# Optimization experiments

Hardware: AMD Instinct MI355X
Metric: run time of the kernel (lower is better)

The kernel has to match this reference:

```python
import jax, jax.numpy as jnp
import numpy as np

D_MODEL = 1024
N_HEADS = 16
D_HIDDEN = 4096
EPS = 1e-6
MASK_VAL = 1e10


def layernorm(x, gamma, beta):
    # Matches torch module: unbiased std (N-1), divide by (std + eps)
    mean = jnp.mean(x, axis=-1, keepdims=True)
    d = x.shape[-1]
    std = jnp.sqrt(jnp.sum((x - mean) ** 2, axis=-1, keepdims=True) / (d - 1))
    return gamma * (x - mean) / (std + EPS) + beta


def multihead(q_in, k_in, v_in, wq, wk, wv, wo, causal):
    # nn.Linear(bias=False): y = x @ W.T
    q = q_in @ wq.T
    k = k_in @ wk.T
    v = v_in @ wv.T
    B, Sq, D = q.shape
    Sk = k.shape[1]
    H, dh = N_HEADS, D // N_HEADS
    q = q.reshape(B, Sq, H, dh)
    k = k.reshape(B, Sk, H, dh)
    v = v.reshape(B, Sk, H, dh)
    scores = jnp.einsum('bqhd,bkhd->bhqk', q, k)  # [B,H,Sq,Sk]
    if causal:
        tri = jnp.triu(jnp.full((Sk, Sk), MASK_VAL, dtype=scores.dtype), k=1)
        scores = scores - tri  # mask applied BEFORE scaling, as in source
    scale = jnp.sqrt(jnp.asarray(D_MODEL, dtype=scores.dtype))  # d_key = d_model
    att = jax.nn.softmax(scores / scale, axis=-1)
    out = jnp.einsum('bhqk,bkhd->bqhd', att, v).reshape(B, Sq, D)
    return out @ wo.T


def setup_inputs() -> dict:
    key = jax.random.key(0)
    ks = jax.random.split(key, 24)
    B, S, D, DH = 2, 2048, D_MODEL, D_HIDDEN
    w = lambda k, shp: (jax.random.normal(k, shp, dtype=jnp.float32) * 0.02)
    inp = {
        'x': jax.random.normal(ks[0], (B, S, D), dtype=jnp.float32),
        'encoding': jax.random.normal(ks[1], (B, S, D), dtype=jnp.float32),
        'sa_wq': w(ks[2], (D, D)), 'sa_wk': w(ks[3], (D, D)),
        'sa_wv': w(ks[4], (D, D)), 'sa_wo': w(ks[5], (D, D)),
        'ca_wq': w(ks[6], (D, D)), 'ca_wk': w(ks[7], (D, D)),
        'ca_wv': w(ks[8], (D, D)), 'ca_wo': w(ks[9], (D, D)),
        'ff_w1': w(ks[10], (DH, D)), 'ff_b1': jnp.zeros((DH,), jnp.float32),
        'ff_w2': w(ks[11], (D, DH)), 'ff_b2': jnp.zeros((D,), jnp.float32),
        'ln1_g': jnp.ones((D,), jnp.float32), 'ln1_b': jnp.zeros((D,), jnp.float32),
        'ln2_g': jnp.ones((D,), jnp.float32), 'ln2_b': jnp.zeros((D,), jnp.float32),
        'ln3_g': jnp.ones((D,), jnp.float32), 'ln3_b': jnp.zeros((D,), jnp.float32),
    }
    return inp


def reference(x, encoding, sa_wq, sa_wk, sa_wv, sa_wo, ca_wq, ca_wk, ca_wv, ca_wo,
              ff_w1, ff_b1, ff_w2, ff_b2, ln1_g, ln1_b, ln2_g, ln2_b, ln3_g, ln3_b):
    # self-attention (causal) + post-norm residual
    h = layernorm(x + multihead(x, x, x, sa_wq, sa_wk, sa_wv, sa_wo, causal=True), ln1_g, ln1_b)
    # cross-attention + post-norm residual
    h = layernorm(h + multihead(h, encoding, encoding, ca_wq, ca_wk, ca_wv, ca_wo, causal=False), ln2_g, ln2_b)
    # feed-forward + post-norm residual
    ff = jax.nn.relu(h @ ff_w1.T + ff_b1) @ ff_w2.T + ff_b2
    return layernorm(h + ff, ln3_g, ln3_b)
```

## Files before the change

### kernel.cpp

```cpp
#include <hip/hip_runtime.h>
#include <hip/hip_bf16.h>
#include <math.h>

#define D_MODEL 1024
#define NHEADS  16
#define DHEAD   64
#define D_HID   4096

typedef __attribute__((ext_vector_type(8))) short short8;
typedef __attribute__((ext_vector_type(4))) short short4v;
typedef __attribute__((ext_vector_type(4))) float f32x4;
typedef __attribute__((ext_vector_type(16))) float f32x16;

#define QSCALE_F 0.04508422002778011f
#define MASK_T   4.5084220e8f

__device__ inline short f2bs(float x) {
    union { __hip_bfloat16 b; short s; } u;
    u.b = __float2bfloat16(x);
    return u.s;
}
__device__ inline float bs2f(ushort s) {
    union { unsigned u; float f; } v; v.u = ((unsigned)s) << 16; return v.f;
}
__device__ inline unsigned cvtpk(float lo, float hi) {
    unsigned r;
    asm("v_cvt_pk_bf16_f32 %0, %1, %2" : "=v"(r) : "v"(lo), "v"(hi));
    return r;
}
__device__ inline short8 pack8(float4 x, float4 y) {
    short8 v;
    v[0] = f2bs(x.x); v[1] = f2bs(x.y); v[2] = f2bs(x.z); v[3] = f2bs(x.w);
    v[4] = f2bs(y.x); v[5] = f2bs(y.y); v[6] = f2bs(y.z); v[7] = f2bs(y.w);
    return v;
}
typedef const unsigned __attribute__((address_space(1))) gu32;
typedef unsigned __attribute__((address_space(3))) lu32;
__device__ inline void gload16(const void* g, void* l) {
    __builtin_amdgcn_global_load_lds((gu32*)g, (lu32*)l, 16, 0, 0);
}
__device__ inline int swz(int r, int byteInRow) {
    return (r * 128 + byteInRow) ^ ((r & 7) << 4);
}

struct WP { const float* p[10]; };
__global__ __launch_bounds__(256) void cast_weights(WP wp, short* __restrict__ dst) {
    const int n8 = (16 << 20) / 8;
    for (int i = blockIdx.x * 256 + threadIdx.x; i < n8; i += gridDim.x * 256) {
        size_t e = (size_t)i * 8;
        int seg = (int)(e >> 20);
        const float* src;
        if (seg < 8)       src = wp.p[seg] + (e & ((1u << 20) - 1));
        else if (seg < 12) src = wp.p[8] + (e - ((size_t)8 << 20));
        else               src = wp.p[9] + (e - ((size_t)12 << 20));
        float4 a = *(const float4*)src;
        float4 b = *(const float4*)(src + 4);
        *(short8*)(dst + e) = pack8(a, b);
    }
}

__global__ __launch_bounds__(256) void cast_f2b(const float* __restrict__ in,
                                                short* __restrict__ out, int n8) {
    for (int i = blockIdx.x * 256 + threadIdx.x; i < n8; i += gridDim.x * 256) {
        float4 a = *(const float4*)(in + (size_t)i * 8);
        float4 b = *(const float4*)(in + (size_t)i * 8 + 4);
        *(short8*)(out + (size_t)i * 8) = pack8(a, b);
    }
}

template<int OM, bool BIAS, bool RELU, bool ACCUM>
__global__ __launch_bounds__(256) void gemm_mfma(
    const short* __restrict__ A, int lda,
    const short* __restrict__ Bm, int ldb,
    const float* __restrict__ bias,
    float* __restrict__ Cf, short* __restrict__ Cb, int ldc,
    int M, int N, int K, size_t routeElems, float qscale)
{
    __shared__ short Als[128 * 64];
    __shared__ short Bls[128 * 64];

    const int tid = threadIdx.x, w = tid >> 6, l = tid & 63;
    const int l15 = l & 15, lhi = l >> 4;
    const int wr = w >> 1, wc = w & 1;

    const int kh = (OM == 3) ? blockIdx.z : 0;
    if (OM == 3) {
        A  += (size_t)kh * K;
        Bm += (size_t)kh * K;
    }

    const unsigned nwg  = gridDim.x * gridDim.y;
    const unsigned wgid = blockIdx.y * gridDim.x + blockIdx.x;
    const unsigned cpx  = nwg >> 3;
    const unsigned sid  = (wgid & 7) * cpx + (wgid >> 3);
    const int bm = (int)(sid / gridDim.x) * 128;
    const int bn = (int)(sid % gridDim.x) * 128;

    const int srow = w * 8 + (l >> 3);
    const int schk = ((l & 7) ^ (l >> 3)) * 8;

    f32x4 acc[4][4] = {};

    for (int k0 = 0; k0 < K; k0 += 64) {
        #pragma unroll
        for (int i = 0; i < 4; ++i) {
            const short* ga = A  + (size_t)(bm + i * 32 + srow) * lda + k0 + schk;
            const short* gb = Bm + (size_t)(bn + i * 32 + srow) * ldb + k0 + schk;
            gload16(ga, &Als[i * 2048 + w * 512]);
            gload16(gb, &Bls[i * 2048 + w * 512]);
        }
        __syncthreads();

        short8 af[4][2], bf[4][2];
        #pragma unroll
        for (int m = 0; m < 4; ++m) {
            const int row = wr * 64 + m * 16 + l15;
            #pragma unroll
            for (int kk = 0; kk < 2; ++kk)
                af[m][kk] = *(const short8*)&Als[row * 64 + (((kk * 4 + lhi) ^ (l15 & 7)) * 8)];
        }
        #pragma unroll
        for (int n = 0; n < 4; ++n) {
            const int row = wc * 64 + n * 16 + l15;
            #pragma unroll
            for (int kk = 0; kk < 2; ++kk)
                bf[n][kk] = *(const short8*)&Bls[row * 64 + (((kk * 4 + lhi) ^ (l15 & 7)) * 8)];
        }
        #pragma unroll
        for (int kk = 0; kk < 2; ++kk)
            #pragma unroll
            for (int m = 0; m < 4; ++m)
                #pragma unroll
                for (int n = 0; n < 4; ++n)
                    acc[m][n] = __builtin_amdgcn_mfma_f32_16x16x32_bf16(af[m][kk], bf[n][kk], acc[m][n], 0, 0, 0);
        __syncthreads();
    }

    #pragma unroll
    for (int n = 0; n < 4; ++n) {
        const int col = bn + wc * 64 + n * 16 + l15;
        float bv = 0.f;
        if (BIAS && (OM != 3 || kh == 0)) bv = bias[col];
        const float sc = (OM == 2) ? (col < 1024 ? qscale : 1.f) : qscale;
        #pragma unroll
        for (int m = 0; m < 4; ++m) {
            const int row0 = bm + wr * 64 + m * 16 + lhi * 4;
            #pragma unroll
            for (int i = 0; i < 4; ++i) {
                float v = acc[m][n][i] + bv;
                if (ACCUM) v += Cf[(size_t)(row0 + i) * ldc + col];
                if (RELU)  v = fmaxf(v, 0.f);
                v *= sc;
                if (OM == 0) {
                    Cf[(size_t)(row0 + i) * ldc + col] = v;
                } else if (OM == 1) {
                    Cb[(size_t)(row0 + i) * ldc + col] = f2bs(v);
                } else if (OM == 2) {
                    Cb[(size_t)(col >> 10) * routeElems +
                       (size_t)(row0 + i) * 1024 + (col & 1023)] = f2bs(v);
                } else {
                    if (kh == 0) Cf[(size_t)(row0 + i) * ldc + col] = v;
                    else         Cb[(size_t)(row0 + i) * ldc + col] = f2bs(v);
                }
            }
        }
    }
}

__global__ __launch_bounds__(256) void v_prep(
    const short* __restrict__ Vb_, short* __restrict__ Vt, int S)
{
    const int t = blockIdx.x, bh = blockIdx.y;
    const int b = bh >> 4, h = bh & 15;
    const int tid = threadIdx.x;
    const int r = tid >> 2, g = tid & 3;
    __shared__ ushort vs[64][65];

    const size_t inrow = ((size_t)b * S + t * 64 + r) * D_MODEL + h * DHEAD;
    const size_t tbase = ((size_t)bh * (S / 64) + t) * 4096;

    short8 v0 = *(const short8*)(Vb_ + inrow + g * 16);
    short8 v1 = *(const short8*)(Vb_ + inrow + g * 16 + 8);
    #pragma unroll
    for (int j = 0; j < 8; ++j) { vs[r][g * 16 + j] = (ushort)v0[j]; vs[r][g * 16 + 8 + j] = (ushort)v1[j]; }
    __syncthreads();
    short8 q0, q1;
    #pragma unroll
    for (int j = 0; j < 8; ++j) {
        q0[j] = (short)vs[g * 16 + j][r];
        q1[j] = (short)vs[g * 16 + 8 + j][r];
    }
    *(short8*)(Vt + tbase + r * 64 + g * 16)     = q0;
    *(short8*)(Vt + tbase + r * 64 + g * 16 + 8) = q1;
}

template<bool CAUSAL>
__global__ __launch_bounds__(256, 3) void attn_v8(
    const short* __restrict__ Qb, const short* __restrict__ Kr,
    const short* __restrict__ Vt, short* __restrict__ PO,
    float* __restrict__ PL, int S)
{
    __shared__ __align__(16) char smem[2 * 16384];

    const int tid = threadIdx.x, w = tid >> 6, l = tid & 63;
    const int l31 = l & 31, hi = l >> 5;
    const int bnd = blockIdx.x >> 1, s = blockIdx.x & 1;
    const int bh = blockIdx.y, b = bh >> 4, h = bh & 15;
    const int qw = bnd * 128 + w * 32;
    const int q  = qw + l31;

    const short* qp = Qb + ((size_t)(b * S + q)) * 1024 + h * 64 + hi * 8;
    short8 bq[4];
    #pragma unroll
    for (int dc = 0; dc < 4; ++dc) bq[dc] = *(const short8*)(qp + dc * 16);

    const short* kbase = Kr + ((size_t)b * S) * 1024 + h * 64;
    const short* vbase = Vt + (size_t)bh * ((S / 64) * 4096);

    f32x16 ot0 = {}, ot1 = {};
    float l_lane = 0.f;

    const int tMax = CAUSAL ? (2 * bnd + 1) : (S / 64 - 1);
    const int sr = tid >> 2, sc = tid & 3;

    short8 gk0, gk1, gv0, gv1;
    {
        const short* kg = kbase + (size_t)(s * 64 + sr) * 1024 + sc * 8;
        const short* vg = vbase + (size_t)s * 4096 + sr * 64 + sc * 8;
        gk0 = *(const short8*)kg;        gk1 = *(const short8*)(kg + 32);
        gv0 = *(const short8*)vg;        gv1 = *(const short8*)(vg + 32);
    }
    {
        char* Kls = smem;            char* Vls = smem + 8192;
        *(short8*)(Kls + swz(sr, sc * 16))      = gk0;
        *(short8*)(Kls + swz(sr, sc * 16 + 64)) = gk1;
        *(short8*)(Vls + swz(sr, sc * 16))      = gv0;
        *(short8*)(Vls + swz(sr, sc * 16 + 64)) = gv1;
    }
    __syncthreads();

    int cur = 0;
    for (int t = s; t <= tMax; t += 2) {
        const bool hasNext = (t + 2 <= tMax);
        if (hasNext) {
            const short* kg = kbase + (size_t)((t + 2) * 64 + sr) * 1024 + sc * 8;
            const short* vg = vbase + (size_t)(t + 2) * 4096 + sr * 64 + sc * 8;
            gk0 = *(const short8*)kg;    gk1 = *(const short8*)(kg + 32);
            gv0 = *(const short8*)vg;    gv1 = *(const short8*)(vg + 32);
        }

        const char* Kls = smem + cur * 16384;
        const char* Vls = Kls + 8192;
        const int kv0 = t * 64;

        if (!(CAUSAL && kv0 > qw + 31)) {
            f32x16 st0 = {}, st1 = {};
            __builtin_amdgcn_s_setprio(1);
            #pragma unroll
            for (int dc = 0; dc < 4; ++dc) {
                short8 a0 = *(const short8*)(Kls + swz(l31,      dc * 32 + hi * 16));
                short8 a1 = *(const short8*)(Kls + swz(32 + l31, dc * 32 + hi * 16));
                st0 = __builtin_amdgcn_mfma_f32_32x32x16_bf16(a0, bq[dc], st0, 0, 0, 0);
                st1 = __builtin_amdgcn_mfma_f32_32x32x16_bf16(a1, bq[dc], st1, 0, 0, 0);
            }
            __builtin_amdgcn_s_setprio(0);

            if (CAUSAL && kv0 + 31 > qw) {
                #pragma unroll
                for (int r = 0; r < 16; ++r) {
                    int kv = kv0 + (r & 3) + 8 * (r >> 2) + 4 * hi;
                    if (kv > q) st0[r] -= MASK_T;
                }
            }
            if (CAUSAL && kv0 + 63 > qw) {
                #pragma unroll
                for (int r = 0; r < 16; ++r) {
                    int kv = kv0 + 32 + (r & 3) + 8 * (r >> 2) + 4 * hi;
                    if (kv > q) st1[r] -= MASK_T;
                }
            }

            union U { unsigned u[4]; short8 s; };
            U c00, c01, c10, c11;
            {
                float p[16];
                #pragma unroll
                for (int r = 0; r < 16; ++r) { p[r] = __builtin_amdgcn_exp2f(st0[r]); l_lane += p[r]; }
                unsigned wd[8], sx[8];
                #pragma unroll
                for (int i = 0; i < 8; ++i) wd[i] = cvtpk(p[2 * i], p[2 * i + 1]);
                #pragma unroll
                for (int i = 0; i < 8; ++i) sx[i] = __shfl_xor(wd[i], 32, 64);
                if (hi == 0) {
                    c00.u[0] = wd[0]; c00.u[1] = wd[1]; c00.u[2] = sx[0]; c00.u[3] = sx[1];
                    c01.u[0] = wd[4]; c01.u[1] = wd[5]; c01.u[2] = sx[4]; c01.u[3] = sx[5];
                } else {
                    c00.u[0] = sx[2]; c00.u[1] = sx[3]; c00.u[2] = wd[2]; c00.u[3] = wd[3];
                    c01.u[0] = sx[6]; c01.u[1] = sx[7]; c01.u[2] = wd[6]; c01.u[3] = wd[7];
                }
            }
            {
                float p[16];
                #pragma unroll
                for (int r = 0; r < 16; ++r) { p[r] = __builtin_amdgcn_exp2f(st1[r]); l_lane += p[r]; }
                unsigned wd[8], sx[8];
                #pragma unroll
                for (int i = 0; i < 8; ++i) wd[i] = cvtpk(p[2 * i], p[2 * i + 1]);
                #pragma unroll
                for (int i = 0; i < 8; ++i) sx[i] = __shfl_xor(wd[i], 32, 64);
                if (hi == 0) {
                    c10.u[0] = wd[0]; c10.u[1] = wd[1]; c10.u[2] = sx[0]; c10.u[3] = sx[1];
                    c11.u[0] = wd[4]; c11.u[1] = wd[5]; c11.u[2] = sx[4]; c11.u[3] = sx[5];
                } else {
                    c10.u[0] = sx[2]; c10.u[1] = sx[3]; c10.u[2] = wd[2]; c10.u[3] = wd[3];
                    c11.u[0] = sx[6]; c11.u[1] = sx[7]; c11.u[2] = wd[6]; c11.u[3] = wd[7];
                }
            }

            __builtin_amdgcn_s_setprio(1);
            short8 av;
            av  = *(const short8*)(Vls + swz(l31,      hi * 16));
            ot0 = __builtin_amdgcn_mfma_f32_32x32x16_bf16(av, c00.s, ot0, 0, 0, 0);
            av  = *(const short8*)(Vls + swz(32 + l31, hi * 16));
            ot1 = __builtin_amdgcn_mfma_f32_32x32x16_bf16(av, c00.s, ot1, 0, 0, 0);
            av  = *(const short8*)(Vls + swz(l31,      32 + hi * 16));
            ot0 = __builtin_amdgcn_mfma_f32_32x32x16_bf16(av, c01.s, ot0, 0, 0, 0);
            av  = *(const short8*)(Vls + swz(32 + l31, 32 + hi * 16));
            ot1 = __builtin_amdgcn_mfma_f32_32x32x16_bf16(av, c01.s, ot1, 0, 0, 0);
            av  = *(const short8*)(Vls + swz(l31,      64 + hi * 16));
            ot0 = __builtin_amdgcn_mfma_f32_32x32x16_bf16(av, c10.s, ot0, 0, 0, 0);
            av  = *(const short8*)(Vls + swz(32 + l31, 64 + hi * 16));
            ot1 = __builtin_amdgcn_mfma_f32_32x32x16_bf16(av, c10.s, ot1, 0, 0, 0);
            av  = *(const short8*)(Vls + swz(l31,      96 + hi * 16));
            ot0 = __builtin_amdgcn_mfma_f32_32x32x16_bf16(av, c11.s, ot0, 0, 0, 0);
            av  = *(const short8*)(Vls + swz(32 + l31, 96 + hi * 16));
            ot1 = __builtin_amdgcn_mfma_f32_32x32x16_bf16(av, c11.s, ot1, 0, 0, 0);
            __builtin_amdgcn_s_setprio(0);
        }

        if (hasNext) {
            char* Kn = smem + (cur ^ 1) * 16384;
            char* Vn = Kn + 8192;
            *(short8*)(Kn + swz(sr, sc * 16))      = gk0;
            *(short8*)(Kn + swz(sr, sc * 16 + 64)) = gk1;
            *(short8*)(Vn + swz(sr, sc * 16))      = gv0;
            *(short8*)(Vn + swz(sr, sc * 16 + 64)) = gv1;
        }
        __syncthreads();
        cur ^= 1;
    }

    const int qc = bnd * 4 + w;
    const size_t c = ((size_t)bh * (S / 32) + qc) * 2 + s;
    float l_tot = l_lane + __shfl_xor(l_lane, 32, 64);
    if (hi == 0) PL[c * 32 + l31] = l_tot;
    short* po = PO + c * 2048 + (size_t)l31 * 64;
    #pragma unroll
    for (int i = 0; i < 8; ++i) {
        int dbase = ((2 * i) & 3) + 8 * (i >> 1) + 4 * hi;
        *(unsigned*)(po + dbase)      = cvtpk(ot0[2 * i], ot0[2 * i + 1]);
        *(unsigned*)(po + 32 + dbase) = cvtpk(ot1[2 * i], ot1[2 * i + 1]);
    }
}

__global__ __launch_bounds__(256) void attn_combine(
    const short* __restrict__ PO, const float* __restrict__ PL,
    short* __restrict__ Out, int S)
{
    const int qc = blockIdx.x, bh = blockIdx.y;
    const int b = bh >> 4, h = bh & 15;
    const size_t cbase = ((size_t)bh * (S / 32) + qc) * 2;
    const int tid = threadIdx.x;
    const int q = tid >> 3, dg = (tid & 7) * 8;

    float den = PL[cbase * 32 + q] + PL[(cbase + 1) * 32 + q];
    float acc[8] = {};
    #pragma unroll
    for (int s = 0; s < 2; ++s) {
        short8 po = *(const short8*)(PO + (cbase + s) * 2048 + q * 64 + dg);
        #pragma unroll
        for (int j = 0; j < 8; ++j) acc[j] += bs2f((ushort)po[j]);
    }
    float inv = 1.f / den;
    short8 o;
    #pragma unroll
    for (int j = 0; j < 8; ++j) o[j] = f2bs(acc[j] * inv);
    *(short8*)(Out + ((size_t)b * S + qc * 32 + q) * 1024 + h * 64 + dg) = o;
}

template<bool IN1BF, bool OUTBF, bool P3>
__global__ __launch_bounds__(256) void add_ln(
    const void* __restrict__ in1, const float* __restrict__ in2,
    const short* __restrict__ in3,
    const float* __restrict__ gam, const float* __restrict__ bet,
    void* __restrict__ y)
{
    const int row = blockIdx.x;
    const int tid = threadIdx.x;
    const size_t off = (size_t)row * D_MODEL;

    float a0, a1, a2, a3;
    if (IN1BF) {
        short4v xs = ((const short4v*)((const short*)in1 + off))[tid];
        a0 = bs2f((ushort)xs[0]); a1 = bs2f((ushort)xs[1]);
        a2 = bs2f((ushort)xs[2]); a3 = bs2f((ushort)xs[3]);
    } else {
        float4 xv = ((const float4*)((const float*)in1 + off))[tid];
        a0 = xv.x; a1 = xv.y; a2 = xv.z; a3 = xv.w;
    }
    float4 rv = ((const float4*)(in2 + off))[tid];
    float v0 = a0 + rv.x, v1 = a1 + rv.y, v2 = a2 + rv.z, v3 = a3 + rv.w;
    if (P3) {
        short4v ps = ((const short4v*)(in3 + off))[tid];
        v0 += bs2f((ushort)ps[0]); v1 += bs2f((ushort)ps[1]);
        v2 += bs2f((ushort)ps[2]); v3 += bs2f((ushort)ps[3]);
    }

    float s  = v0 + v1 + v2 + v3;
    float ss = v0 * v0 + v1 * v1 + v2 * v2 + v3 * v3;

    __shared__ float sb[8];
    #pragma unroll
    for (int o = 32; o > 0; o >>= 1) {
        s  += __shfl_down(s, o, 64);
        ss += __shfl_down(ss, o, 64);
    }
    const int lane = tid & 63, w = tid >> 6;
    if (lane == 0) { sb[w] = s; sb[4 + w] = ss; }
    __syncthreads();
    float S  = sb[0] + sb[1] + sb[2] + sb[3];
    float SS = sb[4] + sb[5] + sb[6] + sb[7];

    float mean = S * (1.f / D_MODEL);
    float var_sum = SS - S * mean;
    float stdv = sqrtf(var_sum * (1.f / (D_MODEL - 1)));
    float inv = 1.f / (stdv + 1e-6f);

    float4 gv = ((const float4*)gam)[tid];
    float4 bv = ((const float4*)bet)[tid];
    float o0 = gv.x * (v0 - mean) * inv + bv.x;
    float o1 = gv.y * (v1 - mean) * inv + bv.y;
    float o2 = gv.z * (v2 - mean) * inv + bv.z;
    float o3 = gv.w * (v3 - mean) * inv + bv.w;
    if (OUTBF) {
        short4v ov; ov[0] = f2bs(o0); ov[1] = f2bs(o1); ov[2] = f2bs(o2); ov[3] = f2bs(o3);
        ((short4v*)((short*)y + off))[tid] = ov;
    } else {
        ((float4*)((float*)y + off))[tid] = make_float4(o0, o1, o2, o3);
    }
}

extern "C" void kernel_launch(void* const* d_in, const int* in_sizes, int n_in,
                              void* d_out, int out_size, void* d_ws, size_t ws_size,
                              hipStream_t stream)
{
    const float* x     = (const float*)d_in[0];
    const float* enc   = (const float*)d_in[1];
    WP wp;
    for (int i = 0; i < 8; ++i) wp.p[i] = (const float*)d_in[2 + i];
    wp.p[8] = (const float*)d_in[10];
    wp.p[9] = (const float*)d_in[12];
    const float* ff_b1 = (const float*)d_in[11];
    const float* ff_b2 = (const float*)d_in[13];
    const float* ln1_g = (const float*)d_in[14];
    const float* ln1_b = (const float*)d_in[15];
    const float* ln2_g = (const float*)d_in[16];
    const float* ln2_b = (const float*)d_in[17];
    const float* ln3_g = (const float*)d_in[18];
    const float* ln3_b = (const float*)d_in[19];
    float* out = (float*)d_out;

    const int Bn = 2, S = 2048, M = Bn * S;
    const size_t MB = 1u << 20;
    char* ws = (char*)d_ws;
    short* Wb   = (short*)(ws);
    short* p32  = (short*)(ws + 32 * MB);
    short* p40  = (short*)(ws + 40 * MB);
    short* p48  = (short*)(ws + 48 * MB);
    short* p56  = (short*)(ws + 56 * MB);
    short* p64  = (short*)(ws + 64 * MB);
    short* p72  = (short*)(ws + 72 * MB);
    float* f0   = (float*)(ws + 80 * MB);

    short* PO  = (short*)f0;
    float* PLl = (float*)p64;
    short* tbuf = p48;

    const size_t RT = 4 * MB;
    const short* W_saqkv = Wb;
    const short* W_sawo  = Wb + 3 * MB;
    const short* W_caq   = Wb + 4 * MB;
    const short* W_cakv  = Wb + 5 * MB;
    const short* W_cawo  = Wb + 7 * MB;
    const short* W_ff1   = Wb + 8 * MB;
    const short* W_ff2   = Wb + 12 * MB;

    dim3 blk(256);
    dim3 g_qkv(3072 / 128, M / 128);
    dim3 g_kv(2048 / 128, M / 128);
    dim3 g_n1k(1024 / 128, M / 128);
    dim3 g_spl(1024 / 128, M / 128, 2);
    dim3 g_ff1(4096 / 128, M / 128);
    dim3 g_attn((S / 128) * 2, Bn * NHEADS);
    dim3 g_cmb(S / 32, Bn * NHEADS);
    dim3 g_vp(S / 64, Bn * NHEADS);
    dim3 g_ln(M);

    cast_weights<<<2048, blk, 0, stream>>>(wp, Wb);
    cast_f2b<<<2048, blk, 0, stream>>>(x, p32, (M * D_MODEL) / 8);

    gemm_mfma<2,false,false,false><<<g_qkv, blk, 0, stream>>>(p32, 1024, W_saqkv, 1024, nullptr, nullptr, p40, 1024, M, 3072, 1024, RT, QSCALE_F);
    v_prep<<<g_vp, blk, 0, stream>>>(p56, p72, S);
    attn_v8<true><<<g_attn, blk, 0, stream>>>(p40, p48, p72, PO, PLl, S);
    attn_combine<<<g_cmb, blk, 0, stream>>>(PO, PLl, p32, S);
    gemm_mfma<3,false,false,false><<<g_spl, blk, 0, stream>>>(p32, 1024, W_sawo, 1024, nullptr, f0, p48, 1024, M, 1024, 512, 0, 1.f);
    add_ln<false,true,true><<<g_ln, blk, 0, stream>>>(x, f0, p48, ln1_g, ln1_b, p32);

    cast_f2b<<<2048, blk, 0, stream>>>(enc, p64, (M * D_MODEL) / 8);
    gemm_mfma<2,false,false,false><<<g_kv, blk, 0, stream>>>(p64, 1024, W_cakv, 1024, nullptr, nullptr, p48, 1024, M, 2048, 1024, RT, 1.f);
    gemm_mfma<1,false,false,false><<<g_n1k, blk, 0, stream>>>(p32, 1024, W_caq, 1024, nullptr, nullptr, p40, 1024, M, 1024, 1024, 0, QSCALE_F);
    v_prep<<<g_vp, blk, 0, stream>>>(p56, p72, S);
    attn_v8<false><<<g_attn, blk, 0, stream>>>(p40, p48, p72, PO, PLl, S);
    attn_combine<<<g_cmb, blk, 0, stream>>>(PO, PLl, p56, S);
    gemm_mfma<3,false,false,false><<<g_spl, blk, 0, stream>>>(p56, 1024, W_cawo, 1024, nullptr, f0, p48, 1024, M, 1024, 512, 0, 1.f);
    add_ln<true,true,true><<<g_ln, blk, 0, stream>>>(p32, f0, p48, ln2_g, ln2_b, p40);

    gemm_mfma<1,true,true,false><<<g_ff1, blk, 0, stream>>>(p40, 1024, W_ff1, 1024, ff_b1, nullptr, tbuf, 4096, M, 4096, 1024, 0, 1.f);
    gemm_mfma<3,true,false,false><<<g_spl, blk, 0, stream>>>(tbuf, 4096, W_ff2, 4096, ff_b2, f0, p32, 1024, M, 1024, 2048, 0, 1.f);
    add_ln<true,false,true><<<g_ln, blk, 0, stream>>>(p40, f0, p32, ln3_g, ln3_b, out);
}
```

Baseline: 386.4 us.

## Drop KV-split in attention and fold normalization into kernel epilogue

The attention kernel no longer splits each query block's key range into two interleaved halves processed by separate blocks. Each block now walks all KV tiles, normalizes by the row sum in registers and writes bf16 output directly, so the separate combine kernel and its partial-output and denominator round trip go away. In exchange the grid is half as large, about 512 blocks, and each block's serial loop is twice as long, which can lower occupancy and load balance, especially for causal blocks near the end of the sequence.

```diff
diff --git a/kernel.cpp b/kernel.cpp
--- a/kernel.cpp
+++ b/kernel.cpp
@@ -195,16 +195,15 @@
 }
 
 template<bool CAUSAL>
-__global__ __launch_bounds__(256, 3) void attn_v8(
+__global__ __launch_bounds__(256, 3) void attn_v10(
     const short* __restrict__ Qb, const short* __restrict__ Kr,
-    const short* __restrict__ Vt, short* __restrict__ PO,
-    float* __restrict__ PL, int S)
+    const short* __restrict__ Vt, short* __restrict__ Out, int S)
 {
     __shared__ __align__(16) char smem[2 * 16384];
 
     const int tid = threadIdx.x, w = tid >> 6, l = tid & 63;
     const int l31 = l & 31, hi = l >> 5;
-    const int bnd = blockIdx.x >> 1, s = blockIdx.x & 1;
+    const int bnd = blockIdx.x;
     const int bh = blockIdx.y, b = bh >> 4, h = bh & 15;
     const int qw = bnd * 128 + w * 32;
     const int q  = qw + l31;
@@ -225,8 +224,8 @@
 
     short8 gk0, gk1, gv0, gv1;
     {
-        const short* kg = kbase + (size_t)(s * 64 + sr) * 1024 + sc * 8;
-        const short* vg = vbase + (size_t)s * 4096 + sr * 64 + sc * 8;
+        const short* kg = kbase + (size_t)(sr) * 1024 + sc * 8;
+        const short* vg = vbase + sr * 64 + sc * 8;
         gk0 = *(const short8*)kg;        gk1 = *(const short8*)(kg + 32);
         gv0 = *(const short8*)vg;        gv1 = *(const short8*)(vg + 32);
     }
@@ -240,11 +239,11 @@
     __syncthreads();
 
     int cur = 0;
-    for (int t = s; t <= tMax; t += 2) {
-        const bool hasNext = (t + 2 <= tMax);
+    for (int t = 0; t <= tMax; ++t) {
+        const bool hasNext = (t + 1 <= tMax);
         if (hasNext) {
-            const short* kg = kbase + (size_t)((t + 2) * 64 + sr) * 1024 + sc * 8;
-            const short* vg = vbase + (size_t)(t + 2) * 4096 + sr * 64 + sc * 8;
+            const short* kg = kbase + (size_t)((t + 1) * 64 + sr) * 1024 + sc * 8;
+            const short* vg = vbase + (size_t)(t + 1) * 4096 + sr * 64 + sc * 8;
             gk0 = *(const short8*)kg;    gk1 = *(const short8*)(kg + 32);
             gv0 = *(const short8*)vg;    gv1 = *(const short8*)(vg + 32);
         }
@@ -350,42 +349,15 @@
         cur ^= 1;
     }
 
-    const int qc = bnd * 4 + w;
-    const size_t c = ((size_t)bh * (S / 32) + qc) * 2 + s;
-    float l_tot = l_lane + __shfl_xor(l_lane, 32, 64);
-    if (hi == 0) PL[c * 32 + l31] = l_tot;
-    short* po = PO + c * 2048 + (size_t)l31 * 64;
+    const float l_tot = l_lane + __shfl_xor(l_lane, 32, 64);
+    const float inv = 1.f / l_tot;
+    short* orow = Out + ((size_t)(b * S + q)) * 1024 + h * 64;
     #pragma unroll
     for (int i = 0; i < 8; ++i) {
         int dbase = ((2 * i) & 3) + 8 * (i >> 1) + 4 * hi;
-        *(unsigned*)(po + dbase)      = cvtpk(ot0[2 * i], ot0[2 * i + 1]);
-        *(unsigned*)(po + 32 + dbase) = cvtpk(ot1[2 * i], ot1[2 * i + 1]);
-    }
-}
-
-__global__ __launch_bounds__(256) void attn_combine(
-    const short* __restrict__ PO, const float* __restrict__ PL,
-    short* __restrict__ Out, int S)
-{
-    const int qc = blockIdx.x, bh = blockIdx.y;
-    const int b = bh >> 4, h = bh & 15;
-    const size_t cbase = ((size_t)bh * (S / 32) + qc) * 2;
-    const int tid = threadIdx.x;
-    const int q = tid >> 3, dg = (tid & 7) * 8;
-
-    float den = PL[cbase * 32 + q] + PL[(cbase + 1) * 32 + q];
-    float acc[8] = {};
-    #pragma unroll
-    for (int s = 0; s < 2; ++s) {
-        short8 po = *(const short8*)(PO + (cbase + s) * 2048 + q * 64 + dg);
-        #pragma unroll
-        for (int j = 0; j < 8; ++j) acc[j] += bs2f((ushort)po[j]);
-    }
-    float inv = 1.f / den;
-    short8 o;
-    #pragma unroll
-    for (int j = 0; j < 8; ++j) o[j] = f2bs(acc[j] * inv);
-    *(short8*)(Out + ((size_t)b * S + qc * 32 + q) * 1024 + h * 64 + dg) = o;
+        *(unsigned*)(orow + dbase)      = cvtpk(ot0[2 * i] * inv, ot0[2 * i + 1] * inv);
+        *(unsigned*)(orow + 32 + dbase) = cvtpk(ot1[2 * i] * inv, ot1[2 * i + 1] * inv);
+    }
 }
 
 template<bool IN1BF, bool OUTBF, bool P3>
@@ -482,8 +454,6 @@
     short* p72  = (short*)(ws + 72 * MB);
     float* f0   = (float*)(ws + 80 * MB);
 
-    short* PO  = (short*)f0;
-    float* PLl = (float*)p64;
     short* tbuf = p48;
 
     const size_t RT = 4 * MB;
@@ -501,8 +471,7 @@
     dim3 g_n1k(1024 / 128, M / 128);
     dim3 g_spl(1024 / 128, M / 128, 2);
     dim3 g_ff1(4096 / 128, M / 128);
-    dim3 g_attn((S / 128) * 2, Bn * NHEADS);
-    dim3 g_cmb(S / 32, Bn * NHEADS);
+    dim3 g_attn(S / 128, Bn * NHEADS);
     dim3 g_vp(S / 64, Bn * NHEADS);
     dim3 g_ln(M);
 
@@ -511,8 +480,7 @@
 
     gemm_mfma<2,false,false,false><<<g_qkv, blk, 0, stream>>>(p32, 1024, W_saqkv, 1024, nullptr, nullptr, p40, 1024, M, 3072, 1024, RT, QSCALE_F);
     v_prep<<<g_vp, blk, 0, stream>>>(p56, p72, S);
-    attn_v8<true><<<g_attn, blk, 0, stream>>>(p40, p48, p72, PO, PLl, S);
-    attn_combine<<<g_cmb, blk, 0, stream>>>(PO, PLl, p32, S);
+    attn_v10<true><<<g_attn, blk, 0, stream>>>(p40, p48, p72, p32, S);
     gemm_mfma<3,false,false,false><<<g_spl, blk, 0, stream>>>(p32, 1024, W_sawo, 1024, nullptr, f0, p48, 1024, M, 1024, 512, 0, 1.f);
     add_ln<false,true,true><<<g_ln, blk, 0, stream>>>(x, f0, p48, ln1_g, ln1_b, p32);
 
@@ -520,8 +488,7 @@
     gemm_mfma<2,false,false,false><<<g_kv, blk, 0, stream>>>(p64, 1024, W_cakv, 1024, nullptr, nullptr, p48, 1024, M, 2048, 1024, RT, 1.f);
     gemm_mfma<1,false,false,false><<<g_n1k, blk, 0, stream>>>(p32, 1024, W_caq, 1024, nullptr, nullptr, p40, 1024, M, 1024, 1024, 0, QSCALE_F);
     v_prep<<<g_vp, blk, 0, stream>>>(p56, p72, S);
-    attn_v8<false><<<g_attn, blk, 0, stream>>>(p40, p48, p72, PO, PLl, S);
-    attn_combine<<<g_cmb, blk, 0, stream>>>(PO, PLl, p56, S);
+    attn_v10<false><<<g_attn, blk, 0, stream>>>(p40, p48, p72, p56, S);
     gemm_mfma<3,false,false,false><<<g_spl, blk, 0, stream>>>(p56, 1024, W_cawo, 1024, nullptr, f0, p48, 1024, M, 1024, 512, 0, 1.f);
     add_ln<true,true,true><<<g_ln, blk, 0, stream>>>(p32, f0, p48, ln2_g, ln2_b, p40);
 
```

Result: faster. 374.6 us (-3.0%).
